# Performance work log

Hardware: AMD Instinct MI355X
Metric: run time of the kernel (lower is better)

## Reference

```python
import jax, jax.numpy as jnp
import numpy as np

B, S, H, L = 4, 2048, 1024, 4
CLAMP_LO, CLAMP_HI = 1e-8, 1.0 - 1e-8
LN_EPS = 1e-5


def setup_inputs() -> dict:
    key = jax.random.key(0)
    ks = jax.random.split(key, 13)
    s = 1.0 / np.sqrt(H)
    u = lambda k, shape: jax.random.uniform(k, shape, jnp.float32, -s, s)
    return {
        "x": jax.random.normal(ks[0], (B, S, H), jnp.float32),
        "fwd_Wz": u(ks[1], (L, H, H)), "fwd_bz": u(ks[2], (L, H)),
        "fwd_Wh": u(ks[3], (L, H, H)), "fwd_bh": u(ks[4], (L, H)),
        "bwd_Wz": u(ks[5], (L, H, H)), "bwd_bz": u(ks[6], (L, H)),
        "bwd_Wh": u(ks[7], (L, H, H)), "bwd_bh": u(ks[8], (L, H)),
        "fusion_W": u(ks[9], (H, 2 * H)), "fusion_b": u(ks[10], (H,)),
        "ln_gamma": jnp.ones((H,), jnp.float32),
        "ln_beta": jnp.zeros((H,), jnp.float32),
    }


def _linear_scan(a, b):
    # h_t = a_t * h_{t-1} + b_t over axis 1 (seq), via associative scan.
    # composition: (a2,b2) o (a1,b1) = (a2*a1, a2*b1 + b2)
    def combine(left, right):
        al, bl = left
        ar, br = right
        return (ar * al, ar * bl + br)
    _, h = jax.lax.associative_scan(combine, (a, b), axis=1)
    return h


def _mingru(x, Wz, bz, Wh, bh):
    # x: (B,S,H); Wz,Wh: (H_out,H_in) like nn.Linear
    z = jax.nn.sigmoid(jnp.einsum('bsi,hi->bsh', x, Wz) + bz)
    h_tilde = jnp.tanh(jnp.einsum('bsi,hi->bsh', x, Wh) + bh)
    a = jnp.clip(1.0 - z, CLAMP_LO, CLAMP_HI)
    return _linear_scan(a, z * h_tilde)


def _layernorm(x, gamma, beta):
    mu = jnp.mean(x, axis=-1, keepdims=True)
    var = jnp.mean(jnp.square(x - mu), axis=-1, keepdims=True)
    return (x - mu) * jax.lax.rsqrt(var + LN_EPS) * gamma + beta


def _stack(x, Wz, bz, Wh, bh, gamma, beta):
    h = x
    for i in range(L):
        h_new = _mingru(h, Wz[i], bz[i], Wh[i], bh[i])
        if i > 0:
            h_new = h_new + h  # residual (shapes match for i>0)
        h = _layernorm(h_new, gamma, beta)
    return h


def reference(x, fwd_Wz, fwd_bz, fwd_Wh, fwd_bh,
              bwd_Wz, bwd_bz, bwd_Wh, bwd_bh,
              fusion_W, fusion_b, ln_gamma, ln_beta):
    h_fwd = _stack(x, fwd_Wz, fwd_bz, fwd_Wh, fwd_bh, ln_gamma, ln_beta)
    h_bwd = _stack(jnp.flip(x, axis=1), bwd_Wz, bwd_bz, bwd_Wh, bwd_bh,
                   ln_gamma, ln_beta)
    h_bwd = jnp.flip(h_bwd, axis=1)
    h_comb = jnp.concatenate([h_fwd, h_bwd], axis=-1)  # (B,S,2H)
    return jnp.einsum('bsi,hi->bsh', h_comb, fusion_W) + fusion_b
```

## Files before the change

kernel.cpp:

```cpp
#include <hip/hip_runtime.h>
#include <stdint.h>

#define Bn 4
#define Sn 2048
#define Hn 1024
#define Ln 4
#define Mn (Bn*Sn)
#define CHUNK 32
#define NCH (Sn/CHUNK)

typedef __bf16 bf16x8 __attribute__((ext_vector_type(8)));
typedef float  f32x4  __attribute__((ext_vector_type(4)));
typedef uint32_t u32;

__device__ __forceinline__ unsigned short f2bf(float f) {
  uint32_t u = __float_as_uint(f);
  uint32_t r = (u + 0x7FFFu + ((u >> 16) & 1u)) >> 16;
  return (unsigned short)r;
}
__device__ __forceinline__ float bf2f(unsigned short u) {
  return __uint_as_float(((uint32_t)u) << 16);
}

__device__ __forceinline__ void gload_lds16(const void* g, void* l) {
  __builtin_amdgcn_global_load_lds((const __attribute__((address_space(1))) void*)g,
                                   (__attribute__((address_space(3))) void*)l, 16, 0, 0);
}

__device__ __forceinline__ void gate_ab(float zp, float hp, float& a, float& bv) {
  float z  = 1.0f / (1.0f + __expf(-zp));
  float e  = __expf(-2.0f * fabsf(hp));
  float th = (1.0f - e) / (1.0f + e);
  th = (hp >= 0.0f) ? th : -th;
  a  = fminf(fmaxf(1.0f - z, 1e-8f), 1.0f - 1e-8f);
  bv = z * th;
}

__global__ __launch_bounds__(256) void cast_all(
    const float* __restrict__ s0, const float* __restrict__ s1,
    const float* __restrict__ s2, const float* __restrict__ s3,
    const float* __restrict__ s4, const float* __restrict__ s5,
    unsigned short* __restrict__ d0, unsigned short* __restrict__ d1,
    unsigned short* __restrict__ d2, unsigned short* __restrict__ d3,
    unsigned short* __restrict__ d4, unsigned short* __restrict__ d5) {
  long i = (long)blockIdx.x * 256 + threadIdx.x;
  const float* s; unsigned short* d; long off;
  if      (i < 1048576) { s = s0; d = d0; off = i; }
  else if (i < 2097152) { s = s1; d = d1; off = i - 1048576; }
  else if (i < 3145728) { s = s2; d = d2; off = i - 2097152; }
  else if (i < 4194304) { s = s3; d = d3; off = i - 3145728; }
  else if (i < 4718592) { s = s4; d = d4; off = i - 4194304; }
  else                  { s = s5; d = d5; off = i - 4718592; }
  float4 v = reinterpret_cast<const float4*>(s)[off];
  ushort4 o;
  o.x = f2bf(v.x); o.y = f2bf(v.y); o.z = f2bf(v.z); o.w = f2bf(v.w);
  reinterpret_cast<ushort4*>(d)[off] = o;
}


#define DSR(d, b, imm) \
  asm volatile("ds_read_b128 %0, %1 offset:%c2" : "=&v"(d) : "v"(b), "i"(imm))

#define VMW(n) do { \
    asm volatile("s_waitcnt vmcnt(" #n ")"); \
    __builtin_amdgcn_sched_barrier(0); \
  } while (0)

#define LGKM(n) do { \
    asm volatile("s_waitcnt lgkmcnt(" #n ")"); \
    __builtin_amdgcn_sched_barrier(0); \
  } while (0)

#define DSRA4(ARR, off) do { \
    DSR(ARR[0], baseA, (off)); \
    DSR(ARR[1], baseA, (off) + 1024); \
    DSR(ARR[2], baseA, (off) + 2048); \
    DSR(ARR[3], baseA, (off) + 3072); \
  } while (0)

#define DSRB4(ARR, off) do { \
    DSR(ARR[0], baseB, (off)); \
    DSR(ARR[1], baseB, (off) + 1024); \
    DSR(ARR[2], baseB, (off) + OB2); \
    DSR(ARR[3], baseB, (off) + OB3); \
  } while (0)

#define CL(ARR, BARR, MB) do { \
    __builtin_amdgcn_s_setprio(1); \
    _Pragma("unroll") \
    for (int _m = 0; _m < 4; ++_m) { \
      _Pragma("unroll") \
      for (int _n = 0; _n < 4; ++_n) \
        acc[(MB) + _m][_n] = __builtin_amdgcn_mfma_f32_16x16x32_bf16( \
            ARR[_m], BARR[_n], acc[(MB) + _m][_n], 0, 0, 0); \
    } \
    __builtin_amdgcn_s_setprio(0); \
  } while (0)

#define BODY(buf) do { \
    if constexpr (MF == 8) { \
      DSRA4(aA, ((buf) * 2 + 0) * RGA); \
      DSRB4(b0, ((buf) * 2 + 0) * 16384); \
      DSRA4(aB, ((buf) * 2 + 0) * RGA + 4096); \
      LGKM(4); \
      CL(aA, b0, 0); \
      DSRB4(b1, ((buf) * 2 + 1) * 16384); \
      LGKM(4); \
      CL(aB, b0, 4); \
      DSRA4(aA, ((buf) * 2 + 1) * RGA); \
      LGKM(4); \
      DSRA4(aB, ((buf) * 2 + 1) * RGA + 4096); \
      LGKM(4); \
      CL(aA, b1, 0); \
      LGKM(0); \
      CL(aB, b1, 4); \
    } else { \
      DSRA4(aA, ((buf) * 2 + 0) * RGA); \
      DSRB4(b0, ((buf) * 2 + 0) * 16384); \
      DSRA4(aB, ((buf) * 2 + 1) * RGA); \
      LGKM(4); \
      CL(aA, b0, 0); \
      DSRB4(b1, ((buf) * 2 + 1) * 16384); \
      LGKM(0); \
      CL(aB, b1, 0); \
    } \
  } while (0)

template<int MF, bool GATE>
__global__ __launch_bounds__(512, 2) void gemm_t(
    const unsigned short* __restrict__ act,
    const unsigned short* __restrict__ Wlo,
    const unsigned short* __restrict__ Whi,
    const float* __restrict__ bias0, const float* __restrict__ bias1,
    int Nsplit, float* __restrict__ out, unsigned short* __restrict__ outbf,
    int Ndim, int K) {
  constexpr int BMR = MF * 32;
  constexpr int RGA = BMR * 64;
  constexpr int OB2 = GATE ? 8192 : 2048;
  constexpr int OB3 = GATE ? 9216 : 3072;
  __shared__ unsigned char smA[4 * RGA];
  __shared__ unsigned char smB[65536];
  const int tid  = threadIdx.x;
  const int lane = tid & 63;
  const int w    = tid >> 6;
  const int waveM = w >> 2;
  const int waveN = w & 3;
  const int bm = blockIdx.x, bn = blockIdx.y;

  const int swz  = (((lane >> 4) ^ ((lane >> 1) & 3)) << 4);
  const int aoff = (waveM * (MF * 16) + (lane & 15)) * 64 + swz;
  const int boff = ((GATE ? waveN * 32 : waveN * 64) + (lane & 15)) * 64 + swz;

  const u32 baseA = (u32)(size_t)(void*)&smA[0] + (u32)aoff;
  const u32 baseB = (u32)(size_t)(void*)&smB[0] + (u32)boff;

  const int srow = tid >> 2;
  const int slog = (tid & 3) ^ ((srow >> 1) & 3);
  const unsigned short* aS0 = act + (size_t)(bm * BMR + srow) * K + slog * 8;
  const unsigned short* aS1 = aS0 + (size_t)128 * K;
  const unsigned short *bS0, *bS1;
  if constexpr (GATE) {
    bS0 = Wlo + (size_t)(bn * 128 + srow) * K + slog * 8;
    bS1 = Whi + (size_t)(bn * 128 + srow) * K + slog * 8;
  } else {
    const unsigned short* Wp; int nbase;
    if (bn * 256 < Nsplit) { Wp = Wlo; nbase = bn * 256; }
    else                   { Wp = Whi; nbase = bn * 256 - Nsplit; }
    bS0 = Wp + (size_t)(nbase + srow) * K + slog * 8;
    bS1 = bS0 + (size_t)128 * K;
  }
  const int wB = w * 1024;

  f32x4 acc[MF][4];
#pragma unroll
  for (int m = 0; m < MF; ++m)
#pragma unroll
    for (int n = 0; n < 4; ++n) acc[m][n] = (f32x4)0.0f;

  bf16x8 aA[4], aB[4], b0[4], b1[4];

  auto STG4 = [&](int t, int buf) {
#pragma unroll
    for (int kh = 0; kh < 2; ++kh) {
      unsigned char* ra = smA + (buf * 2 + kh) * RGA;
      gload_lds16(aS0 + (size_t)t * 64 + kh * 32, ra + wB);
      if constexpr (MF == 8)
        gload_lds16(aS1 + (size_t)t * 64 + kh * 32, ra + 8192 + wB);
      unsigned char* rb = smB + (buf * 2 + kh) * 16384;
      gload_lds16(bS0 + (size_t)t * 64 + kh * 32, rb + wB);
      gload_lds16(bS1 + (size_t)t * 64 + kh * 32, rb + 8192 + wB);
    }
  };

  const int nkt   = K >> 6;
  const int niter = nkt >> 1;

  STG4(0, 0);
  VMW(0);
  __builtin_amdgcn_s_barrier();

  for (int j = 0; j < niter - 1; ++j) {
    STG4(2 * j + 1, 1); BODY(0); VMW(0); __builtin_amdgcn_s_barrier();
    STG4(2 * j + 2, 0); BODY(1); VMW(0); __builtin_amdgcn_s_barrier();
  }
  STG4(nkt - 1, 1); BODY(0); VMW(0); __builtin_amdgcn_s_barrier();
  BODY(1);

  const int rowBase = bm * BMR + waveM * (MF * 16);
  if constexpr (GATE) {
#pragma unroll
    for (int n = 0; n < 2; ++n) {
      const int col = bn * 128 + waveN * 32 + n * 16 + (lane & 15);
      const float bz = bias0[col];
      const float bh = bias1[col];
#pragma unroll
      for (int m = 0; m < MF; ++m) {
#pragma unroll
        for (int r = 0; r < 4; ++r) {
          int row = rowBase + m * 16 + (lane >> 4) * 4 + r;
          float a, bv;
          gate_ab(acc[m][n][r] + bz, acc[m][n + 2][r] + bh, a, bv);
          outbf[(size_t)row * 2048 + col]        = f2bf(a);
          outbf[(size_t)row * 2048 + 1024 + col] = f2bf(bv);
        }
      }
    }
  } else {
    const int colBase = bn * 256 + waveN * 64;
#pragma unroll
    for (int m = 0; m < MF; ++m) {
#pragma unroll
      for (int n = 0; n < 4; ++n) {
        int col = colBase + n * 16 + (lane & 15);
        float bv = (col < Nsplit) ? bias0[col] : bias1[col - Nsplit];
        if (outbf) {
#pragma unroll
          for (int r = 0; r < 4; ++r) {
            int row = rowBase + m * 16 + (lane >> 4) * 4 + r;
            outbf[(size_t)row * Ndim + col] = f2bf(acc[m][n][r] + bv);
          }
        } else {
#pragma unroll
          for (int r = 0; r < 4; ++r) {
            int row = rowBase + m * 16 + (lane >> 4) * 4 + r;
            out[(size_t)row * Ndim + col] = acc[m][n][r] + bv;
          }
        }
      }
    }
  }
}

__global__ __launch_bounds__(256) void scan_p1(const unsigned short* __restrict__ pre,
                                               float* __restrict__ Ac, float* __restrict__ Bc,
                                               int dir) {
  int tid = threadIdx.x;
  int bid = blockIdx.x;
  int ht = bid & 3;
  int c  = (bid >> 2) & (NCH - 1);
  int b  = bid >> 8;
  int h  = ht * 256 + tid;
  float Aa = 1.0f, Bb = 0.0f;
  for (int j = 0; j < CHUNK; ++j) {
    int t = c * CHUNK + j;
    int s = dir ? (Sn - 1 - t) : t;
    const unsigned short* p = pre + (size_t)(b * Sn + s) * 2048;
    float a  = bf2f(p[h]);
    float bv = bf2f(p[1024 + h]);
    Aa = a * Aa;
    Bb = a * Bb + bv;
  }
  Ac[(size_t)(b * NCH + c) * Hn + h] = Aa;
  Bc[(size_t)(b * NCH + c) * Hn + h] = Bb;
}

__global__ __launch_bounds__(1024) void scan_p3_ln(
    const unsigned short* __restrict__ pre,
    const float* __restrict__ Ac, const float* __restrict__ Bc,
    const unsigned short* __restrict__ resid,
    const float* __restrict__ gamma, const float* __restrict__ beta,
    unsigned short* __restrict__ out_bf,
    int bf_stride, int bf_off, int dir) {
  __shared__ unsigned short hsl[CHUNK][Hn];
  const int h = threadIdx.x;
  const int c = blockIdx.x & (NCH - 1);
  const int b = blockIdx.x >> 6;

  float hprev = 0.0f;
  {
    int cc = 0;
    for (; cc + 8 <= c; cc += 8) {
      float Af[8], Bf[8];
#pragma unroll
      for (int q = 0; q < 8; ++q) {
        size_t idx = (size_t)(b * NCH + cc + q) * Hn + h;
        Af[q] = Ac[idx];
        Bf[q] = Bc[idx];
      }
#pragma unroll
      for (int q = 0; q < 8; ++q) hprev = Af[q] * hprev + Bf[q];
    }
    for (; cc < c; ++cc) {
      size_t idx = (size_t)(b * NCH + cc) * Hn + h;
      hprev = Ac[idx] * hprev + Bc[idx];
    }
  }

  for (int j = 0; j < CHUNK; ++j) {
    int t = c * CHUNK + j;
    int s = dir ? (Sn - 1 - t) : t;
    const unsigned short* p = pre + (size_t)(b * Sn + s) * 2048;
    float a  = bf2f(p[h]);
    float bv = bf2f(p[1024 + h]);
    hprev = a * hprev + bv;
    hsl[j][h] = f2bf(hprev);
  }
  __syncthreads();

  const int lane = h & 63;
  const int wv   = h >> 6;
  float gm[16], bt[16];
  {
    const float4* gp = reinterpret_cast<const float4*>(gamma);
    const float4* bp = reinterpret_cast<const float4*>(beta);
#pragma unroll
    for (int half = 0; half < 2; ++half) {
      int base = half * 128 + lane * 2;
#pragma unroll
      for (int i = 0; i < 2; ++i) {
        float4 g4 = gp[base + i], b4 = bp[base + i];
        int o = half * 8 + i * 4;
        gm[o+0] = g4.x; gm[o+1] = g4.y; gm[o+2] = g4.z; gm[o+3] = g4.w;
        bt[o+0] = b4.x; bt[o+1] = b4.y; bt[o+2] = b4.z; bt[o+3] = b4.w;
      }
    }
  }

  for (int rr = 0; rr < 2; ++rr) {
    const int j = wv * 2 + rr;
    const int t = c * CHUNK + j;
    const int s = dir ? (Sn - 1 - t) : t;
    const size_t row = (size_t)(b * Sn + s);

    const uint4* rp = reinterpret_cast<const uint4*>(&hsl[j][0]);
    uint4 q0 = rp[lane], q1 = rp[64 + lane];
    uint32_t uw[8] = {q0.x, q0.y, q0.z, q0.w, q1.x, q1.y, q1.z, q1.w};
    float v[16];
#pragma unroll
    for (int k = 0; k < 8; ++k) {
      v[2*k]   = bf2f((unsigned short)(uw[k] & 0xffffu));
      v[2*k+1] = bf2f((unsigned short)(uw[k] >> 16));
    }
    if (resid) {
      const uint4* rf = reinterpret_cast<const uint4*>(resid + row * Hn);
      uint4 r0v = rf[lane], r1v = rf[64 + lane];
      uint32_t rw[8] = {r0v.x, r0v.y, r0v.z, r0v.w, r1v.x, r1v.y, r1v.z, r1v.w};
#pragma unroll
      for (int k = 0; k < 8; ++k) {
        v[2*k]   += bf2f((unsigned short)(rw[k] & 0xffffu));
        v[2*k+1] += bf2f((unsigned short)(rw[k] >> 16));
      }
    }
    float s1 = 0.0f, s2 = 0.0f;
#pragma unroll
    for (int m = 0; m < 16; ++m) { s1 += v[m]; s2 += v[m] * v[m]; }
#pragma unroll
    for (int off = 1; off < 64; off <<= 1) {
      s1 += __shfl_xor(s1, off);
      s2 += __shfl_xor(s2, off);
    }
    float mu  = s1 * (1.0f / Hn);
    float var = s2 * (1.0f / Hn) - mu * mu;
    float rs  = rsqrtf(var + 1e-5f);

    float o[16];
#pragma unroll
    for (int m = 0; m < 16; ++m) o[m] = (v[m] - mu) * rs * gm[m] + bt[m];

    uint4* ob = reinterpret_cast<uint4*>(out_bf + row * bf_stride + bf_off);
    uint4 w0, w1;
    w0.x = f2bf(o[0])  | ((u32)f2bf(o[1])  << 16);
    w0.y = f2bf(o[2])  | ((u32)f2bf(o[3])  << 16);
    w0.z = f2bf(o[4])  | ((u32)f2bf(o[5])  << 16);
    w0.w = f2bf(o[6])  | ((u32)f2bf(o[7])  << 16);
    w1.x = f2bf(o[8])  | ((u32)f2bf(o[9])  << 16);
    w1.y = f2bf(o[10]) | ((u32)f2bf(o[11]) << 16);
    w1.z = f2bf(o[12]) | ((u32)f2bf(o[13]) << 16);
    w1.w = f2bf(o[14]) | ((u32)f2bf(o[15]) << 16);
    ob[lane]      = w0;
    ob[64 + lane] = w1;
  }
}

extern "C" void kernel_launch(void* const* d_in, const int* in_sizes, int n_in,
                              void* d_out, int out_size, void* d_ws, size_t ws_size,
                              hipStream_t stream) {
  const float* x        = (const float*)d_in[0];
  const float* fwd_Wz   = (const float*)d_in[1];
  const float* fwd_bz   = (const float*)d_in[2];
  const float* fwd_Wh   = (const float*)d_in[3];
  const float* fwd_bh   = (const float*)d_in[4];
  const float* bwd_Wz   = (const float*)d_in[5];
  const float* bwd_bz   = (const float*)d_in[6];
  const float* bwd_Wh   = (const float*)d_in[7];
  const float* bwd_bh   = (const float*)d_in[8];
  const float* fusion_W = (const float*)d_in[9];
  const float* fusion_b = (const float*)d_in[10];
  const float* gamma    = (const float*)d_in[11];
  const float* beta     = (const float*)d_in[12];
  float* out = (float*)d_out;

  unsigned short* WzA    = (unsigned short*)d_ws;
  unsigned short* WhA    = WzA + 8ULL * 1024 * 1024;
  unsigned short* fusWbf = WhA + 8ULL * 1024 * 1024;
  unsigned short* xbf    = fusWbf + 2ULL * 1024 * 1024;
  unsigned short* actbf  = xbf + 8ULL * 1024 * 1024;
  unsigned short* combbf = actbf + 8ULL * 1024 * 1024;
  float* actf = (float*)(combbf + 16ULL * 1024 * 1024);
  float* pre  = actf + 8ULL * 1024 * 1024;
  float* hs   = pre + 16ULL * 1024 * 1024;
  float* Ac   = hs + 8ULL * 1024 * 1024;
  float* Bc   = Ac + (size_t)Bn * NCH * Hn;
  float* pref = Bc + (size_t)Bn * NCH * Hn;
  size_t need = (size_t)((char*)(pref + (size_t)Bn * NCH * Hn) - (char*)d_ws);
  if (ws_size < need) return;
  unsigned short* prebf = (unsigned short*)pre;

  cast_all<<<26624, 256, 0, stream>>>(
      fwd_Wz, bwd_Wz, fwd_Wh, bwd_Wh, fusion_W, x,
      WzA, WzA + 4ULL * 1024 * 1024, WhA, WhA + 4ULL * 1024 * 1024, fusWbf, xbf);

  for (int d = 0; d < 2; ++d) {
    const float* bz = d ? bwd_bz : fwd_bz;
    const float* bh = d ? bwd_bh : fwd_bh;
    for (int l = 0; l < Ln; ++l) {
      const unsigned short* a_in = (l == 0) ? xbf : actbf;
      const unsigned short* Wlo = WzA + (size_t)(d * 4 + l) * 1024 * 1024;
      const unsigned short* Whi = WhA + (size_t)(d * 4 + l) * 1024 * 1024;
      gemm_t<8, true><<<dim3(Mn / 256, 8), 512, 0, stream>>>(
          a_in, Wlo, Whi, bz + l * 1024, bh + l * 1024, 1024,
          nullptr, prebf, 2048, 1024);
      scan_p1<<<Bn * NCH * 4, 256, 0, stream>>>(prebf, Ac, Bc, d);
      if (l < Ln - 1)
        scan_p3_ln<<<Bn * NCH, 1024, 0, stream>>>(
            prebf, Ac, Bc, (l == 0) ? nullptr : actbf, gamma, beta,
            actbf, 1024, 0, d);
      else
        scan_p3_ln<<<Bn * NCH, 1024, 0, stream>>>(
            prebf, Ac, Bc, actbf, gamma, beta,
            combbf, 2048, d * 1024, d);
    }
  }
  gemm_t<4, false><<<dim3(Mn / 128, 1024 / 256), 512, 0, stream>>>(
      combbf, fusWbf, fusWbf, fusion_b, fusion_b, 1 << 30, out, nullptr, 1024, 2048);
}
```

Measured before the change: 599.0 us.

## Fuse chunk-level scan summaries into gate GEMM epilogue, drop scan_p1 kernel

After: 570.9 us. 1.05x faster.

```diff
diff --git a/kernel.cpp b/kernel.cpp
--- a/kernel.cpp
+++ b/kernel.cpp
@@ -133,6 +133,7 @@
     const unsigned short* __restrict__ Whi,
     const float* __restrict__ bias0, const float* __restrict__ bias1,
     int Nsplit, float* __restrict__ out, unsigned short* __restrict__ outbf,
+    float* __restrict__ Acp, float* __restrict__ Bcp, int dir,
     int Ndim, int K) {
   constexpr int BMR = MF * 32;
   constexpr int RGA = BMR * 64;
@@ -208,21 +209,70 @@
 
   const int rowBase = bm * BMR + waveM * (MF * 16);
   if constexpr (GATE) {
-#pragma unroll
-    for (int n = 0; n < 2; ++n) {
-      const int col = bn * 128 + waveN * 32 + n * 16 + (lane & 15);
-      const float bz = bias0[col];
-      const float bh = bias1[col];
-#pragma unroll
-      for (int m = 0; m < MF; ++m) {
+    const int colBase = bn * 128 + waveN * 32;
+    const int c0 = lane & 15;
+    const int q  = lane >> 4;
+    const float bz0 = bias0[colBase + c0],      bh0 = bias1[colBase + c0];
+    const float bz1 = bias0[colBase + 16 + c0], bh1 = bias1[colBase + 16 + c0];
+    const int batch   = bm >> 3;
+    const int schunk0 = (bm & 7) * 8;
+
+#pragma unroll
+    for (int k = 0; k < 4; ++k) {
+      float CA[2][2], CB[2][2];
+#pragma unroll
+      for (int mm = 0; mm < 2; ++mm) {
+        const int m = k * 2 + mm;
+        float TA[2] = {1.0f, 1.0f}, TB[2] = {0.0f, 0.0f};
 #pragma unroll
         for (int r = 0; r < 4; ++r) {
-          int row = rowBase + m * 16 + (lane >> 4) * 4 + r;
-          float a, bv;
-          gate_ab(acc[m][n][r] + bz, acc[m][n + 2][r] + bh, a, bv);
-          outbf[(size_t)row * 2048 + col]        = f2bf(a);
-          outbf[(size_t)row * 2048 + 1024 + col] = f2bf(bv);
+          const int row = rowBase + m * 16 + q * 4 + r;
+          float a0, bv0, a1, bv1;
+          gate_ab(acc[m][0][r] + bz0, acc[m][2][r] + bh0, a0, bv0);
+          gate_ab(acc[m][1][r] + bz1, acc[m][3][r] + bh1, a1, bv1);
+          const unsigned short ua0 = f2bf(a0), ua1 = f2bf(a1);
+          const unsigned short ub0 = f2bf(bv0), ub1 = f2bf(bv1);
+          unsigned short* pr = outbf + (size_t)row * 2048;
+          pr[colBase + c0]             = ua0;
+          pr[colBase + 16 + c0]        = ua1;
+          pr[1024 + colBase + c0]      = ub0;
+          pr[1024 + colBase + 16 + c0] = ub1;
+          const float ra[2] = {bf2f(ua0), bf2f(ua1)};
+          const float rb[2] = {bf2f(ub0), bf2f(ub1)};
+#pragma unroll
+          for (int n = 0; n < 2; ++n) {
+            if (dir == 0) { TB[n] = ra[n] * TB[n] + rb[n]; TA[n] = ra[n] * TA[n]; }
+            else          { TB[n] = TA[n] * rb[n] + TB[n]; TA[n] = TA[n] * ra[n]; }
+          }
         }
+#pragma unroll
+        for (int st = 0; st < 2; ++st) {
+          const int msk = 16 << st;
+          const bool self_later = (dir == 0) ? (((q >> st) & 1) != 0)
+                                             : (((q >> st) & 1) == 0);
+#pragma unroll
+          for (int n = 0; n < 2; ++n) {
+            float pA = __shfl_xor(TA[n], msk);
+            float pB = __shfl_xor(TB[n], msk);
+            if (self_later) { TB[n] = TA[n] * pB + TB[n]; TA[n] = TA[n] * pA; }
+            else            { TB[n] = pA * TB[n] + pB;    TA[n] = pA * TA[n]; }
+          }
+        }
+        CA[mm][0] = TA[0]; CA[mm][1] = TA[1];
+        CB[mm][0] = TB[0]; CB[mm][1] = TB[1];
+      }
+      float FA[2], FB[2];
+#pragma unroll
+      for (int n = 0; n < 2; ++n) {
+        if (dir == 0) { FA[n] = CA[1][n] * CA[0][n]; FB[n] = CA[1][n] * CB[0][n] + CB[1][n]; }
+        else          { FA[n] = CA[0][n] * CA[1][n]; FB[n] = CA[0][n] * CB[1][n] + CB[0][n]; }
+      }
+      const int kk = waveM * 4 + k;
+      const int c  = (dir == 0) ? (schunk0 + kk) : (63 - schunk0 - kk);
+      if (q == 0) {
+        size_t idx = (size_t)(batch * NCH + c) * Hn + colBase + c0;
+        Acp[idx]      = FA[0]; Bcp[idx]      = FB[0];
+        Acp[idx + 16] = FA[1]; Bcp[idx + 16] = FB[1];
       }
     }
   } else {
@@ -249,29 +299,6 @@
       }
     }
   }
-}
-
-__global__ __launch_bounds__(256) void scan_p1(const unsigned short* __restrict__ pre,
-                                               float* __restrict__ Ac, float* __restrict__ Bc,
-                                               int dir) {
-  int tid = threadIdx.x;
-  int bid = blockIdx.x;
-  int ht = bid & 3;
-  int c  = (bid >> 2) & (NCH - 1);
-  int b  = bid >> 8;
-  int h  = ht * 256 + tid;
-  float Aa = 1.0f, Bb = 0.0f;
-  for (int j = 0; j < CHUNK; ++j) {
-    int t = c * CHUNK + j;
-    int s = dir ? (Sn - 1 - t) : t;
-    const unsigned short* p = pre + (size_t)(b * Sn + s) * 2048;
-    float a  = bf2f(p[h]);
-    float bv = bf2f(p[1024 + h]);
-    Aa = a * Aa;
-    Bb = a * Bb + bv;
-  }
-  Ac[(size_t)(b * NCH + c) * Hn + h] = Aa;
-  Bc[(size_t)(b * NCH + c) * Hn + h] = Bb;
 }
 
 __global__ __launch_bounds__(1024) void scan_p3_ln(
@@ -292,13 +319,13 @@
     for (; cc + 8 <= c; cc += 8) {
       float Af[8], Bf[8];
 #pragma unroll
-      for (int q = 0; q < 8; ++q) {
-        size_t idx = (size_t)(b * NCH + cc + q) * Hn + h;
-        Af[q] = Ac[idx];
-        Bf[q] = Bc[idx];
-      }
-#pragma unroll
-      for (int q = 0; q < 8; ++q) hprev = Af[q] * hprev + Bf[q];
+      for (int qq = 0; qq < 8; ++qq) {
+        size_t idx = (size_t)(b * NCH + cc + qq) * Hn + h;
+        Af[qq] = Ac[idx];
+        Bf[qq] = Bc[idx];
+      }
+#pragma unroll
+      for (int qq = 0; qq < 8; ++qq) hprev = Af[qq] * hprev + Bf[qq];
     }
     for (; cc < c; ++cc) {
       size_t idx = (size_t)(b * NCH + cc) * Hn + h;
@@ -439,8 +466,7 @@
       const unsigned short* Whi = WhA + (size_t)(d * 4 + l) * 1024 * 1024;
       gemm_t<8, true><<<dim3(Mn / 256, 8), 512, 0, stream>>>(
           a_in, Wlo, Whi, bz + l * 1024, bh + l * 1024, 1024,
-          nullptr, prebf, 2048, 1024);
-      scan_p1<<<Bn * NCH * 4, 256, 0, stream>>>(prebf, Ac, Bc, d);
+          nullptr, prebf, Ac, Bc, d, 2048, 1024);
       if (l < Ln - 1)
         scan_p3_ln<<<Bn * NCH, 1024, 0, stream>>>(
             prebf, Ac, Bc, (l == 0) ? nullptr : actbf, gamma, beta,
@@ -452,5 +478,6 @@
     }
   }
   gemm_t<4, false><<<dim3(Mn / 128, 1024 / 256), 512, 0, stream>>>(
-      combbf, fusWbf, fusWbf, fusion_b, fusion_b, 1 << 30, out, nullptr, 1024, 2048);
-}
+      combbf, fusWbf, fusWbf, fusion_b, fusion_b, 1 << 30, out, nullptr,
+      nullptr, nullptr, 0, 1024, 2048);
+}
```
